# Optimization experiments

Measured on AMD Instinct MI355X. Metric: run time of the kernel, lower is better.

Reference implementation:

```python
import jax, jax.numpy as jnp
import numpy as np

TEMP = 0.07
LN_EPS = 1e-5


def _l2norm(x, eps=1e-12):
    n = jnp.linalg.norm(x, axis=-1, keepdims=True)
    return x / jnp.maximum(n, eps)


def setup_inputs() -> dict:
    key = jax.random.key(0)
    ks = jax.random.split(key, 8)
    B, N, D, S = 1024, 100000, 1024, 2
    scale = 1.0 / np.sqrt(D)
    return {
        "q": jax.random.normal(ks[0], (B, D), jnp.float32),
        "bank_values": jax.random.normal(ks[1], (N, D), jnp.float32),
        "proj_w": jax.random.normal(ks[2], (S, D, D), jnp.float32) * scale,
        "proj_b": jax.random.normal(ks[3], (S, D), jnp.float32) * 0.01,
        "unify_w": jax.random.normal(ks[4], (S, D, D), jnp.float32) * scale,
        "unify_b": jax.random.normal(ks[5], (S, D), jnp.float32) * 0.01,
        "ln_gamma": jnp.ones((D,), jnp.float32),
        "ln_beta": jnp.zeros((D,), jnp.float32),
        "top_m": 32,
    }


def reference(q, bank_values, proj_w, proj_b, unify_w, unify_b, ln_gamma, ln_beta, top_m):
    # PrototypeBank.build: keys = L2-normalized values (detached)
    keys = _l2norm(bank_values)  # [N, D]
    num_scales = proj_w.shape[0]
    ref = jnp.zeros_like(q)
    for s in range(num_scales):  # small fixed structural loop
        p = q @ proj_w[s].T + proj_b[s]                       # [B, D] Linear
        scores = _l2norm(p) @ keys.T                          # [B, N] cosine
        top_s, top_i = jax.lax.top_k(scores, top_m)           # [B, m]
        attn = jax.nn.softmax(top_s / TEMP, axis=-1)          # [B, m]
        z = jnp.einsum('bm,bmd->bd', attn, bank_values[top_i])  # weighted gather-sum
        ref = ref + z @ unify_w[s].T + unify_b[s]
    mu = ref.mean(axis=-1, keepdims=True)
    var = ref.var(axis=-1, keepdims=True)
    out = (ref - mu) * jax.lax.rsqrt(var + LN_EPS) * ln_gamma + ln_beta
    return out
```

## Files before the change

kernel.cpp:

```cpp
#include <hip/hip_runtime.h>
#include <math.h>


static inline size_t align256(size_t x){ return (x + 255) & ~size_t(255); }

typedef short bf16x8 __attribute__((ext_vector_type(8)));
typedef float f32x4  __attribute__((ext_vector_type(4)));

#define GLOAD_LDS16(gp, lp) \
  __builtin_amdgcn_global_load_lds((const __attribute__((address_space(1))) unsigned int*)(gp), \
                                   (__attribute__((address_space(3))) unsigned int*)(lp), 16, 0, 0)

__device__ inline unsigned short f2bf(float f){
  unsigned int u = __float_as_uint(f);
  u += 0x7fffu + ((u >> 16) & 1u);
  return (unsigned short)(u >> 16);
}

__global__ __launch_bounds__(256) void row_rnorm_kernel(
    const float* __restrict__ X, float* __restrict__ rn, int rows, int D)
{
  int wv = threadIdx.x >> 6, lane = threadIdx.x & 63;
  int r = blockIdx.x * 4 + wv;
  if (r >= rows) return;
  const float4* xr = (const float4*)(X + (size_t)r * D);
  int nv = D >> 2;
  float ss = 0.f;
  for (int i = lane; i < nv; i += 64){
    float4 v = xr[i];
    ss = fmaf(v.x,v.x, fmaf(v.y,v.y, fmaf(v.z,v.z, fmaf(v.w,v.w, ss))));
  }
  #pragma unroll
  for (int off = 32; off; off >>= 1) ss += __shfl_xor(ss, off);
  if (lane == 0) rn[r] = 1.f / fmaxf(sqrtf(ss), 1e-12f);
}

__global__ __launch_bounds__(256) void convert_bf16_kernel(
    const float* __restrict__ X, const float* __restrict__ rowscale,
    unsigned short* __restrict__ out, long total8, int D)
{
  long i = (long)blockIdx.x * 256 + threadIdx.x;
  const long stride = (long)gridDim.x * 256;
  for (; i < total8; i += stride){
    long e = i * 8;
    int r = (int)(e / D);
    float sc = rowscale ? rowscale[r] : 1.f;
    float4 v0 = *(const float4*)(X + e);
    float4 v1 = *(const float4*)(X + e + 4);
    v0.x*=sc; v0.y*=sc; v0.z*=sc; v0.w*=sc;
    v1.x*=sc; v1.y*=sc; v1.z*=sc; v1.w*=sc;
    uint4 w;
    w.x = (unsigned)f2bf(v0.x) | ((unsigned)f2bf(v0.y) << 16);
    w.y = (unsigned)f2bf(v0.z) | ((unsigned)f2bf(v0.w) << 16);
    w.z = (unsigned)f2bf(v1.x) | ((unsigned)f2bf(v1.y) << 16);
    w.w = (unsigned)f2bf(v1.z) | ((unsigned)f2bf(v1.w) << 16);
    *(uint4*)(out + e) = w;
  }
}

template<int RM, int RN, bool ACCUM>
__global__ __launch_bounds__(256) void gemm_nt_kernel(
    const float* __restrict__ A, const float* __restrict__ B,
    const float* __restrict__ bias, const float* __restrict__ bscale,
    float* __restrict__ C, int M, int Nn, int K, int Brows, int ldc)
{
  __shared__ float As[16][RM*64 + 4];
  __shared__ float Bs[16][RN*64 + 4];
  const int t  = threadIdx.x;
  const int tm = t >> 4, tn = t & 15;
  const int m0 = blockIdx.y * (RM*64), n0 = blockIdx.x * (RN*64);

  float acc[RM][RN][4][4];
  #pragma unroll
  for (int r=0;r<RM;++r)
    #pragma unroll
    for (int c=0;c<RN;++c)
      #pragma unroll
      for (int i=0;i<4;++i)
        #pragma unroll
        for (int j=0;j<4;++j) acc[r][c][i][j]=0.f;

  for (int kp = 0; kp < K; kp += 16){
    #pragma unroll
    for (int l = 0; l < RM; ++l){
      int li = t + l*256;
      int row = li >> 2, kq = (li & 3) << 2;
      float4 v = *(const float4*)(A + (size_t)(m0+row)*K + kp + kq);
      As[kq+0][row]=v.x; As[kq+1][row]=v.y; As[kq+2][row]=v.z; As[kq+3][row]=v.w;
    }
    #pragma unroll
    for (int l = 0; l < RN; ++l){
      int li = t + l*256;
      int row = li >> 2, kq = (li & 3) << 2;
      int gn = n0 + row;
      float4 v = make_float4(0.f,0.f,0.f,0.f);
      float sc = 1.f;
      if (gn < Brows){
        v = *(const float4*)(B + (size_t)gn*K + kp + kq);
        if (bscale) sc = bscale[gn];
      }
      Bs[kq+0][row]=v.x*sc; Bs[kq+1][row]=v.y*sc; Bs[kq+2][row]=v.z*sc; Bs[kq+3][row]=v.w*sc;
    }
    __syncthreads();
    #pragma unroll
    for (int kk = 0; kk < 16; ++kk){
      float av[RM][4], bv[RN][4];
      #pragma unroll
      for (int r=0;r<RM;++r){
        float4 a = *(const float4*)&As[kk][r*64 + tm*4];
        av[r][0]=a.x; av[r][1]=a.y; av[r][2]=a.z; av[r][3]=a.w;
      }
      #pragma unroll
      for (int c=0;c<RN;++c){
        float4 b = *(const float4*)&Bs[kk][c*64 + tn*4];
        bv[c][0]=b.x; bv[c][1]=b.y; bv[c][2]=b.z; bv[c][3]=b.w;
      }
      #pragma unroll
      for (int r=0;r<RM;++r)
        #pragma unroll
        for (int c=0;c<RN;++c)
          #pragma unroll
          for (int i=0;i<4;++i)
            #pragma unroll
            for (int j=0;j<4;++j)
              acc[r][c][i][j] = fmaf(av[r][i], bv[c][j], acc[r][c][i][j]);
    }
    __syncthreads();
  }

  #pragma unroll
  for (int r=0;r<RM;++r){
    #pragma unroll
    for (int i=0;i<4;++i){
      int gm = m0 + r*64 + tm*4 + i;
      #pragma unroll
      for (int c=0;c<RN;++c){
        int gn = n0 + c*64 + tn*4;
        if (gn >= Nn) continue;
        float* cp = C + (size_t)gm*ldc + gn;
        float o0=acc[r][c][i][0], o1=acc[r][c][i][1], o2=acc[r][c][i][2], o3=acc[r][c][i][3];
        if (gn + 3 < Nn){
          float4 o = make_float4(o0,o1,o2,o3);
          if (bias){ float4 bb = *(const float4*)&bias[gn]; o.x+=bb.x; o.y+=bb.y; o.z+=bb.z; o.w+=bb.w; }
          if (ACCUM){ float4 cc = *(const float4*)cp; o.x+=cc.x; o.y+=cc.y; o.z+=cc.z; o.w+=cc.w; }
          *(float4*)cp = o;
        } else {
          float ov[4] = {o0,o1,o2,o3};
          for (int j=0;j<4;++j){
            if (gn + j < Nn){
              float o = ov[j];
              if (bias)  o += bias[gn+j];
              if (ACCUM) o += cp[j];
              cp[j] = o;
            }
          }
        }
      }
    }
  }
}

__global__ __launch_bounds__(512, 2) void scores_mfma_kernel(
    const unsigned short* __restrict__ Abf, const unsigned short* __restrict__ Bbf,
    float* __restrict__ C, int M, int Nn, int K, int ldc)
{
  __shared__ __align__(16) unsigned char smem[65536];
  unsigned char* As = smem;
  unsigned char* Bs = smem + 32768;

  const int t = threadIdx.x;
  const int lane = t & 63, wid = t >> 6;
  const int wm = wid >> 2, wn = wid & 3;
  const int l15 = lane & 15, l4 = lane >> 4;
  const int m0 = blockIdx.y * 256, n0 = blockIdx.x * 256;

  f32x4 acc[8][4];
  #pragma unroll
  for (int i=0;i<8;++i)
    #pragma unroll
    for (int j=0;j<4;++j) acc[i][j] = (f32x4)0.f;

  const int srow = t >> 3;
  const int sb   = (t & 7) * 16;
  unsigned char* As_w = As + wid*1024;
  unsigned char* Bs_w = Bs + wid*1024;

  for (int kp = 0; kp < K; kp += 64){
    #pragma unroll
    for (int i = 0; i < 4; ++i){
      int row = srow + i*64;
      int xr  = (row & 7) << 4;
      int src = sb ^ xr;
      const unsigned char* ga = (const unsigned char*)Abf
          + ((size_t)(m0+row)*K + kp)*2 + src;
      GLOAD_LDS16(ga, As_w + i*8192);
      int gn = n0 + row; if (gn >= Nn) gn = Nn - 1;
      const unsigned char* gb = (const unsigned char*)Bbf
          + ((size_t)gn*K + kp)*2 + src;
      GLOAD_LDS16(gb, Bs_w + i*8192);
    }
    __syncthreads();

    bf16x8 B0[4], B1[4];
    #pragma unroll
    for (int fn = 0; fn < 4; ++fn){
      int brow = wn*64 + fn*16 + l15;
      int xr = (brow & 7) << 4;
      const unsigned char* bp = Bs + brow*128;
      B0[fn] = *(const bf16x8*)(bp + (( l4*16      ) ^ xr));
      B1[fn] = *(const bf16x8*)(bp + ((64 + l4*16 ) ^ xr));
    }
    #pragma unroll
    for (int fm = 0; fm < 8; ++fm){
      int arow = wm*128 + fm*16 + l15;
      int xr = (arow & 7) << 4;
      const unsigned char* ap = As + arow*128;
      bf16x8 A0 = *(const bf16x8*)(ap + (( l4*16      ) ^ xr));
      bf16x8 A1 = *(const bf16x8*)(ap + ((64 + l4*16 ) ^ xr));
      #pragma unroll
      for (int fn = 0; fn < 4; ++fn){
        acc[fm][fn] = __builtin_amdgcn_mfma_f32_16x16x32_bf16(A0, B0[fn], acc[fm][fn], 0,0,0);
        acc[fm][fn] = __builtin_amdgcn_mfma_f32_16x16x32_bf16(A1, B1[fn], acc[fm][fn], 0,0,0);
      }
    }
    __syncthreads();
  }

  #pragma unroll
  for (int fm = 0; fm < 8; ++fm){
    int row = m0 + wm*128 + fm*16 + l4*4;
    #pragma unroll
    for (int fn = 0; fn < 4; ++fn){
      int col = n0 + wn*64 + fn*16 + l15;
      if (col < Nn){
        float* cp = C + (size_t)row*ldc + col;
        #pragma unroll
        for (int r = 0; r < 4; ++r) cp[(size_t)r*ldc] = acc[fm][fn][r];
      }
    }
  }
}

__global__ __launch_bounds__(256) void chunk_filter_kernel(
    const float* __restrict__ scores, int ldc, int colbase, int Nwindow,
    int NC, float* __restrict__ cand_s, int* __restrict__ cand_i,
    int chunk0, int nchunks_total, int cap, float eps)
{
  extern __shared__ float lds[];
  __shared__ float sv[256];
  __shared__ float tau_s;
  __shared__ int cnt;
  const int row = blockIdx.x, t = threadIdx.x;
  const int lc = blockIdx.y;
  const int col0l = lc * NC;
  int ncols = Nwindow - col0l; if (ncols > NC) ncols = NC;
  const int gchunk = chunk0 + lc;
  const float* sr = scores + (size_t)row * ldc + col0l;

  float m0 = -INFINITY, m1 = -INFINITY, m2 = -INFINITY, m3 = -INFINITY;
  const int nc4 = ncols >> 2;
  const float4* sr4 = (const float4*)sr;
  float4* lds4 = (float4*)lds;
  for (int j = t; j < nc4; j += 256){
    float4 v = sr4[j];
    lds4[j] = v;
    m0 = fmaxf(m0, v.x); m1 = fmaxf(m1, v.y);
    m2 = fmaxf(m2, v.z); m3 = fmaxf(m3, v.w);
  }
  for (int j = (nc4 << 2) + t; j < ncols; j += 256){
    float v = sr[j];
    lds[j] = v;
    m0 = fmaxf(m0, v);
  }
  sv[t] = fmaxf(fmaxf(m0, m1), fmaxf(m2, m3));
  __syncthreads();

  for (int k = 2; k <= 256; k <<= 1){
    for (int j = k >> 1; j > 0; j >>= 1){
      int p = t ^ j;
      float a = sv[t], b = sv[p];
      bool up = ((t & k) == 0);
      float keep = (t < p) ? (up ? fmaxf(a,b) : fminf(a,b))
                           : (up ? fminf(a,b) : fmaxf(a,b));
      __syncthreads();
      sv[t] = keep;
      __syncthreads();
    }
  }
  if (t == 0){ tau_s = sv[31]; cnt = 0; }
  __syncthreads();
  const float thr = tau_s - eps;

  float* cs = cand_s + ((size_t)row * nchunks_total + gchunk) * cap;
  int*   ci = cand_i + ((size_t)row * nchunks_total + gchunk) * cap;

  for (int j = t; j < ncols; j += 256){
    float v = lds[j];
    if (v >= thr){
      int pos = atomicAdd(&cnt, 1);
      if (pos < cap){ cs[pos] = v; ci[pos] = colbase + col0l + j; }
    }
  }
  __syncthreads();
  int n = cnt < cap ? cnt : cap;
  for (int j = n + t; j < cap; j += 256) ci[j] = -1;
}

__global__ __launch_bounds__(256) void select_softmax_gather_kernel(
    const float* __restrict__ cand_s, const int* __restrict__ cand_i,
    const float* __restrict__ p, const float* __restrict__ rn_bank,
    const float* __restrict__ pnorm, const float* __restrict__ bank,
    float* __restrict__ z, int ncap, int D, int topm, float invtemp, float eps)
{
  __shared__ float p_s[1024];
  __shared__ float vs[1024]; __shared__ int vi[1024];
  __shared__ float sv[256];
  __shared__ int   cidx[256];
  __shared__ float rv[256];
  __shared__ float tau_s;
  __shared__ int cnt;
  const int row = blockIdx.x, t = threadIdx.x;
  const int lane = t & 63, wid = t >> 6;

  const float4* pr = (const float4*)(p + (size_t)row * D);
  for (int i = t; i < (D >> 2); i += 256) ((float4*)p_s)[i] = pr[i];
  const float* cs = cand_s + (size_t)row * ncap;
  const int*  ci = cand_i + (size_t)row * ncap;
  for (int j = t; j < ncap; j += 256){
    int k = ci[j];
    vi[j] = k;
    vs[j] = (k >= 0) ? cs[j] : -INFINITY;
  }
  __syncthreads();

  float m = -INFINITY;
  for (int j = t; j < ncap; j += 256) m = fmaxf(m, vs[j]);
  sv[t] = m;
  __syncthreads();
  for (int k = 2; k <= 256; k <<= 1){
    for (int j = k >> 1; j > 0; j >>= 1){
      int pp = t ^ j;
      float a = sv[t], b = sv[pp];
      bool up = ((t & k) == 0);
      float keep = (t < pp) ? (up ? fmaxf(a,b) : fminf(a,b))
                            : (up ? fminf(a,b) : fmaxf(a,b));
      __syncthreads();
      sv[t] = keep;
      __syncthreads();
    }
  }
  if (t == 0){ tau_s = sv[31]; cnt = 0; }
  __syncthreads();
  const float thr = tau_s - eps;

  for (int j = t; j < ncap; j += 256){
    if (vi[j] >= 0 && vs[j] >= thr){
      int pos = atomicAdd(&cnt, 1);
      if (pos < 256) cidx[pos] = vi[j];
    }
  }
  __syncthreads();
  const int n2 = cnt < 256 ? cnt : 256;
  rv[t] = -INFINITY;
  if (t >= n2) cidx[t] = 0x7fffffff;
  __syncthreads();

  const int nj = D >> 8;
  for (int c = wid; c < n2; c += 4){
    int idx = cidx[c];
    const float4* kr = (const float4*)(bank + (size_t)idx * D);
    float ss = 0.f;
    for (int j = 0; j < nj; ++j){
      float4 kv = kr[lane + j*64];
      float4 pv = *(const float4*)&p_s[(lane + j*64) << 2];
      ss = fmaf(pv.x,kv.x, fmaf(pv.y,kv.y, fmaf(pv.z,kv.z, fmaf(pv.w,kv.w, ss))));
    }
    #pragma unroll
    for (int off = 32; off; off >>= 1) ss += __shfl_xor(ss, off);
    if (lane == 0) rv[c] = ss * rn_bank[idx];
  }
  __syncthreads();

  for (int k = 2; k <= 256; k <<= 1){
    for (int j = k >> 1; j > 0; j >>= 1){
      int pp = t ^ j;
      float av = rv[t];  int ai = cidx[t];
      float bv = rv[pp]; int bi = cidx[pp];
      bool up = ((t & k) == 0);
      bool agtb = (av > bv) || (av == bv && ai < bi);
      bool keepA = (t < pp) ? (up ? agtb : !agtb)
                            : (up ? !agtb : agtb);
      __syncthreads();
      if (keepA){ rv[t] = av; cidx[t] = ai; } else { rv[t] = bv; cidx[t] = bi; }
      __syncthreads();
    }
  }

  if (t == 0){
    float pn = pnorm[row] * invtemp;
    float mx = rv[0] * pn;
    float sum = 0.f;
    for (int i = 0; i < topm; ++i){
      float w = expf(rv[i]*pn - mx);
      sv[i] = w; sum += w;
    }
    float inv = 1.f / sum;
    for (int i = 0; i < topm; ++i) sv[i] *= inv;
  }
  __syncthreads();

  for (int d4 = t; d4 < (D >> 2); d4 += 256){
    float ax=0.f, ay=0.f, az=0.f, aw=0.f;
    for (int i = 0; i < topm; ++i){
      float a = sv[i];
      const float4 v = *(const float4*)(bank + (size_t)cidx[i]*D + (d4<<2));
      ax = fmaf(a, v.x, ax); ay = fmaf(a, v.y, ay);
      az = fmaf(a, v.z, az); aw = fmaf(a, v.w, aw);
    }
    *(float4*)(z + (size_t)row*D + (d4<<2)) = make_float4(ax,ay,az,aw);
  }
}

__global__ __launch_bounds__(256) void layernorm_kernel(
    const float* __restrict__ ref, const float* __restrict__ gamma,
    const float* __restrict__ beta, float* __restrict__ out, int D, float eps)
{
  __shared__ float s1[4], s2[4];
  const int row = blockIdx.x, t = threadIdx.x;
  const float4* xr = (const float4*)(ref + (size_t)row*D);
  int nv = D >> 2;
  float sum = 0.f, ssq = 0.f;
  for (int i = t; i < nv; i += 256){
    float4 v = xr[i];
    sum += v.x+v.y+v.z+v.w;
    ssq = fmaf(v.x,v.x, fmaf(v.y,v.y, fmaf(v.z,v.z, fmaf(v.w,v.w, ssq))));
  }
  const int lane = t & 63, wid = t >> 6;
  #pragma unroll
  for (int off = 32; off; off >>= 1){ sum += __shfl_xor(sum, off); ssq += __shfl_xor(ssq, off); }
  if (lane == 0){ s1[wid] = sum; s2[wid] = ssq; }
  __syncthreads();
  sum = s1[0]+s1[1]+s1[2]+s1[3];
  ssq = s2[0]+s2[1]+s2[2]+s2[3];
  float mu  = sum / (float)D;
  float var = ssq / (float)D - mu*mu;
  float rs  = rsqrtf(var + eps);
  const float4* g4 = (const float4*)gamma;
  const float4* b4 = (const float4*)beta;
  float4* o4 = (float4*)(out + (size_t)row*D);
  for (int i = t; i < nv; i += 256){
    float4 v = xr[i], g = g4[i], bb = b4[i];
    float4 o;
    o.x = (v.x-mu)*rs*g.x + bb.x;
    o.y = (v.y-mu)*rs*g.y + bb.y;
    o.z = (v.z-mu)*rs*g.z + bb.z;
    o.w = (v.w-mu)*rs*g.w + bb.w;
    o4[i] = o;
  }
}

extern "C" void kernel_launch(void* const* d_in, const int* in_sizes, int n_in,
                              void* d_out, int out_size, void* d_ws, size_t ws_size,
                              hipStream_t stream)
{
  const float* q       = (const float*)d_in[0];
  const float* bank    = (const float*)d_in[1];
  const float* proj_w  = (const float*)d_in[2];
  const float* proj_b  = (const float*)d_in[3];
  const float* unify_w = (const float*)d_in[4];
  const float* unify_b = (const float*)d_in[5];
  const float* gamma   = (const float*)d_in[6];
  const float* beta    = (const float*)d_in[7];

  const int D = in_sizes[6];
  const int B = in_sizes[0] / D;
  const int N = in_sizes[1] / D;
  const int S = in_sizes[2] / (D * D);
  const int TOPM = 32;
  const int CAP  = 64;
  const int NC   = 12544;
  const int WCH  = 4;
  const float INVTEMP = 1.0f / 0.07f;
  const float EPS = 0.025f;

  const int NCH = (N + NC - 1) / NC;
  const int SCW = NC * WCH;

  char* wsb = (char*)d_ws;
  size_t off = 0;
  auto take = [&](size_t bytes)->char*{ char* p = wsb + off; off += align256(bytes); return p; };
  float* rn_bank = (float*)take((size_t)N*4);
  float* pnorm   = (float*)take((size_t)B*4);
  float* p       = (float*)take((size_t)B*D*4);
  float* z       = (float*)take((size_t)B*D*4);
  float* ref     = (float*)take((size_t)B*D*4);
  float* cand_s  = (float*)take((size_t)B*NCH*CAP*4);
  int*   cand_i  = (int*)  take((size_t)B*NCH*CAP*4);
  unsigned short* bank_bf = (unsigned short*)take((size_t)N*D*2);
  unsigned short* p_bf    = (unsigned short*)take((size_t)B*D*2);
  float* scores  = (float*)take((size_t)B*(size_t)SCW*4);

  row_rnorm_kernel<<<(N+3)/4, 256, 0, stream>>>(bank, rn_bank, N, D);
  convert_bf16_kernel<<<2048, 256, 0, stream>>>(
      bank, rn_bank, bank_bf, (long)N*D/8, D);

  for (int s = 0; s < S; ++s){
    dim3 g1(D/64, B/64);
    gemm_nt_kernel<1,1,false><<<g1, 256, 0, stream>>>(
        q, proj_w + (size_t)s*D*D, proj_b + (size_t)s*D, nullptr,
        p, B, D, D, D, D);
    row_rnorm_kernel<<<(B+3)/4, 256, 0, stream>>>(p, pnorm, B, D);
    convert_bf16_kernel<<<512, 256, 0, stream>>>(
        p, nullptr, p_bf, (long)B*D/8, D);

    for (int w0 = 0; w0 < N; w0 += SCW){
      int nw = N - w0; if (nw > SCW) nw = SCW;
      dim3 g2((nw + 255)/256, B/256);
      scores_mfma_kernel<<<g2, 512, 0, stream>>>(
          p_bf, bank_bf + (size_t)w0*D,
          scores, B, nw, D, SCW);
      int ncw = (nw + NC - 1) / NC;
      chunk_filter_kernel<<<dim3(B, ncw), 256, (size_t)NC*4, stream>>>(
          scores, SCW, w0, nw, NC, cand_s, cand_i,
          w0 / NC, NCH, CAP, EPS);
    }

    select_softmax_gather_kernel<<<B, 256, 0, stream>>>(
        cand_s, cand_i, p, rn_bank, pnorm, bank, z,
        NCH*CAP, D, TOPM, INVTEMP, EPS);

    if (s == 0)
      gemm_nt_kernel<1,1,false><<<g1, 256, 0, stream>>>(
          z, unify_w + (size_t)s*D*D, unify_b + (size_t)s*D, nullptr,
          ref, B, D, D, D, D);
    else
      gemm_nt_kernel<1,1,true><<<g1, 256, 0, stream>>>(
          z, unify_w + (size_t)s*D*D, unify_b + (size_t)s*D, nullptr,
          ref, B, D, D, D, D);
  }

  layernorm_kernel<<<B, 256, 0, stream>>>(ref, gamma, beta, (float*)d_out, D, 1e-5f);
}
```

Before: 1.694 ms.

## Store scores as bf16 and double-buffer the scores GEMM K-loop

```diff
diff --git a/kernel.cpp b/kernel.cpp
--- a/kernel.cpp
+++ b/kernel.cpp
@@ -15,6 +15,9 @@
   unsigned int u = __float_as_uint(f);
   u += 0x7fffu + ((u >> 16) & 1u);
   return (unsigned short)(u >> 16);
+}
+__device__ inline float bf2f(unsigned int h16){
+  return __uint_as_float(h16 << 16);
 }
 
 __global__ __launch_bounds__(256) void row_rnorm_kernel(
@@ -162,11 +165,9 @@
 
 __global__ __launch_bounds__(512, 2) void scores_mfma_kernel(
     const unsigned short* __restrict__ Abf, const unsigned short* __restrict__ Bbf,
-    float* __restrict__ C, int M, int Nn, int K, int ldc)
+    unsigned short* __restrict__ C, int M, int Nn, int K, int ldc)
 {
   __shared__ __align__(16) unsigned char smem[65536];
-  unsigned char* As = smem;
-  unsigned char* Bs = smem + 32768;
 
   const int t = threadIdx.x;
   const int lane = t & 63, wid = t >> 6;
@@ -180,51 +181,58 @@
     #pragma unroll
     for (int j=0;j<4;++j) acc[i][j] = (f32x4)0.f;
 
-  const int srow = t >> 3;
-  const int sb   = (t & 7) * 16;
-  unsigned char* As_w = As + wid*1024;
-  unsigned char* Bs_w = Bs + wid*1024;
-
-  for (int kp = 0; kp < K; kp += 64){
-    #pragma unroll
-    for (int i = 0; i < 4; ++i){
-      int row = srow + i*64;
-      int xr  = (row & 7) << 4;
-      int src = sb ^ xr;
-      const unsigned char* ga = (const unsigned char*)Abf
-          + ((size_t)(m0+row)*K + kp)*2 + src;
-      GLOAD_LDS16(ga, As_w + i*8192);
-      int gn = n0 + row; if (gn >= Nn) gn = Nn - 1;
-      const unsigned char* gb = (const unsigned char*)Bbf
-          + ((size_t)gn*K + kp)*2 + src;
-      GLOAD_LDS16(gb, Bs_w + i*8192);
+  const int srow = t >> 2;
+  const int sb   = (t & 3) * 16;
+  const int ldsb = wid * 1024;
+
+  const int NT = K >> 5;
+
+  #define STAGE(kp, bufsel)                                                   \
+    {                                                                         \
+      unsigned char* Ab_ = smem + (bufsel)*32768;                             \
+      unsigned char* Bb_ = smem + (bufsel)*32768 + 16384;                     \
+      _Pragma("unroll")                                                       \
+      for (int i_ = 0; i_ < 2; ++i_){                                         \
+        int row_ = srow + i_*128;                                             \
+        int src_ = sb ^ ((row_ & 3) << 4);                                    \
+        const unsigned char* ga_ = (const unsigned char*)Abf                  \
+            + ((size_t)(m0+row_)*K + (kp))*2 + src_;                          \
+        GLOAD_LDS16(ga_, Ab_ + ldsb + i_*8192);                               \
+        int gn_ = n0 + row_; if (gn_ >= Nn) gn_ = Nn - 1;                     \
+        const unsigned char* gb_ = (const unsigned char*)Bbf                  \
+            + ((size_t)gn_*K + (kp))*2 + src_;                                \
+        GLOAD_LDS16(gb_, Bb_ + ldsb + i_*8192);                               \
+      }                                                                       \
+    }
+
+  STAGE(0, 0);
+  __syncthreads();
+
+  int cur = 0;
+  for (int tt = 0; tt < NT; ++tt){
+    if (tt + 1 < NT) STAGE((tt+1) << 5, cur ^ 1);
+
+    const unsigned char* Ab = smem + cur*32768;
+    const unsigned char* Bb = smem + cur*32768 + 16384;
+
+    bf16x8 Bf[4];
+    #pragma unroll
+    for (int fn = 0; fn < 4; ++fn){
+      int br = wn*64 + fn*16 + l15;
+      Bf[fn] = *(const bf16x8*)(Bb + br*64 + ((l4*16) ^ ((br & 3) << 4)));
+    }
+    #pragma unroll
+    for (int fm = 0; fm < 8; ++fm){
+      int ar = wm*128 + fm*16 + l15;
+      bf16x8 Af = *(const bf16x8*)(Ab + ar*64 + ((l4*16) ^ ((ar & 3) << 4)));
+      #pragma unroll
+      for (int fn = 0; fn < 4; ++fn)
+        acc[fm][fn] = __builtin_amdgcn_mfma_f32_16x16x32_bf16(Af, Bf[fn], acc[fm][fn], 0,0,0);
     }
     __syncthreads();
-
-    bf16x8 B0[4], B1[4];
-    #pragma unroll
-    for (int fn = 0; fn < 4; ++fn){
-      int brow = wn*64 + fn*16 + l15;
-      int xr = (brow & 7) << 4;
-      const unsigned char* bp = Bs + brow*128;
-      B0[fn] = *(const bf16x8*)(bp + (( l4*16      ) ^ xr));
-      B1[fn] = *(const bf16x8*)(bp + ((64 + l4*16 ) ^ xr));
-    }
-    #pragma unroll
-    for (int fm = 0; fm < 8; ++fm){
-      int arow = wm*128 + fm*16 + l15;
-      int xr = (arow & 7) << 4;
-      const unsigned char* ap = As + arow*128;
-      bf16x8 A0 = *(const bf16x8*)(ap + (( l4*16      ) ^ xr));
-      bf16x8 A1 = *(const bf16x8*)(ap + ((64 + l4*16 ) ^ xr));
-      #pragma unroll
-      for (int fn = 0; fn < 4; ++fn){
-        acc[fm][fn] = __builtin_amdgcn_mfma_f32_16x16x32_bf16(A0, B0[fn], acc[fm][fn], 0,0,0);
-        acc[fm][fn] = __builtin_amdgcn_mfma_f32_16x16x32_bf16(A1, B1[fn], acc[fm][fn], 0,0,0);
-      }
-    }
-    __syncthreads();
-  }
+    cur ^= 1;
+  }
+  #undef STAGE
 
   #pragma unroll
   for (int fm = 0; fm < 8; ++fm){
@@ -233,16 +241,16 @@
     for (int fn = 0; fn < 4; ++fn){
       int col = n0 + wn*64 + fn*16 + l15;
       if (col < Nn){
-        float* cp = C + (size_t)row*ldc + col;
+        unsigned short* cp = C + (size_t)row*ldc + col;
         #pragma unroll
-        for (int r = 0; r < 4; ++r) cp[(size_t)r*ldc] = acc[fm][fn][r];
+        for (int r = 0; r < 4; ++r) cp[(size_t)r*ldc] = f2bf(acc[fm][fn][r]);
       }
     }
   }
 }
 
 __global__ __launch_bounds__(256) void chunk_filter_kernel(
-    const float* __restrict__ scores, int ldc, int colbase, int Nwindow,
+    const unsigned short* __restrict__ scores, int ldc, int colbase, int Nwindow,
     int NC, float* __restrict__ cand_s, int* __restrict__ cand_i,
     int chunk0, int nchunks_total, int cap, float eps)
 {
@@ -255,20 +263,25 @@
   const int col0l = lc * NC;
   int ncols = Nwindow - col0l; if (ncols > NC) ncols = NC;
   const int gchunk = chunk0 + lc;
-  const float* sr = scores + (size_t)row * ldc + col0l;
+  const unsigned short* sr = scores + (size_t)row * ldc + col0l;
 
   float m0 = -INFINITY, m1 = -INFINITY, m2 = -INFINITY, m3 = -INFINITY;
-  const int nc4 = ncols >> 2;
-  const float4* sr4 = (const float4*)sr;
+  const int nc8 = ncols >> 3;
+  const uint4* sr8 = (const uint4*)sr;
   float4* lds4 = (float4*)lds;
-  for (int j = t; j < nc4; j += 256){
-    float4 v = sr4[j];
-    lds4[j] = v;
-    m0 = fmaxf(m0, v.x); m1 = fmaxf(m1, v.y);
-    m2 = fmaxf(m2, v.z); m3 = fmaxf(m3, v.w);
-  }
-  for (int j = (nc4 << 2) + t; j < ncols; j += 256){
-    float v = sr[j];
+  for (int j = t; j < nc8; j += 256){
+    uint4 v = sr8[j];
+    float4 a = make_float4(bf2f(v.x & 0xffffu), bf2f(v.x >> 16),
+                           bf2f(v.y & 0xffffu), bf2f(v.y >> 16));
+    float4 b = make_float4(bf2f(v.z & 0xffffu), bf2f(v.z >> 16),
+                           bf2f(v.w & 0xffffu), bf2f(v.w >> 16));
+    lds4[j*2]   = a;
+    lds4[j*2+1] = b;
+    m0 = fmaxf(m0, fmaxf(a.x, b.x)); m1 = fmaxf(m1, fmaxf(a.y, b.y));
+    m2 = fmaxf(m2, fmaxf(a.z, b.z)); m3 = fmaxf(m3, fmaxf(a.w, b.w));
+  }
+  for (int j = (nc8 << 3) + t; j < ncols; j += 256){
+    float v = bf2f((unsigned)sr[j]);
     lds[j] = v;
     m0 = fmaxf(m0, v);
   }
@@ -498,7 +511,7 @@
   int*   cand_i  = (int*)  take((size_t)B*NCH*CAP*4);
   unsigned short* bank_bf = (unsigned short*)take((size_t)N*D*2);
   unsigned short* p_bf    = (unsigned short*)take((size_t)B*D*2);
-  float* scores  = (float*)take((size_t)B*(size_t)SCW*4);
+  unsigned short* scores  = (unsigned short*)take((size_t)B*(size_t)SCW*2);
 
   row_rnorm_kernel<<<(N+3)/4, 256, 0, stream>>>(bank, rn_bank, N, D);
   convert_bf16_kernel<<<2048, 256, 0, stream>>>(
```

Result: faster. 1.501 ms (-11.4%).
